# Kernel tuning notes

Hardware: AMD Instinct MI355X
Metric: run time of the kernel (lower is better)

Reference implementation:

```python
import jax, jax.numpy as jnp
import numpy as np

B, S, DIM = 2, 2048, 1024
N_HEAD, HEAD_DIM = 16, 64


def setup_inputs() -> dict:
    key = jax.random.key(0)
    k1, k2, k3, k4 = jax.random.split(key, 4)
    x = jax.random.normal(k1, (B, S, DIM), dtype=jnp.float32)
    # rotary table: cos/sin pairs, shape [S, head_dim//2, 2]
    half = HEAD_DIM // 2
    inv_freq = 1.0 / (10000.0 ** (jnp.arange(0, half, dtype=jnp.float32) / half))
    t = jnp.arange(S, dtype=jnp.float32)
    ang = t[:, None] * inv_freq[None, :]
    freqs_cis = jnp.stack([jnp.cos(ang), jnp.sin(ang)], axis=-1)  # [S, half, 2]
    # causal boolean mask [1,1,S,S] (True = attend)
    mask = jnp.tril(jnp.ones((S, S), dtype=bool))[None, None]
    wqkv = jax.random.normal(k2, (3 * DIM, DIM), dtype=jnp.float32) * (DIM ** -0.5)
    wo = jax.random.normal(k3, (DIM, DIM), dtype=jnp.float32) * (DIM ** -0.5)
    return {"x": x, "freqs_cis": freqs_cis, "mask": mask, "wqkv": wqkv, "wo": wo}


def apply_rotary_emb(x, freqs_cis):
    # x: [B, S, H, D]; freqs_cis: [S, D//2, 2]
    xs = x.reshape(*x.shape[:-1], -1, 2)  # [B,S,H,D//2,2]
    fc = freqs_cis[None, :, None, :, :]  # [1,S,1,D//2,2]
    xr, xi = xs[..., 0], xs[..., 1]
    cr, ci = fc[..., 0], fc[..., 1]
    out = jnp.stack([xr * cr - xi * ci, xi * cr + xr * ci], axis=-1)
    return out.reshape(x.shape)


def reference(x, freqs_cis, mask, wqkv, wo):
    bsz, seqlen, _ = x.shape
    qkv = jnp.einsum('bsd,ed->bse', x, wqkv)  # [B,S,3*dim]
    q, k, v = jnp.split(qkv, 3, axis=-1)
    q = q.reshape(bsz, seqlen, N_HEAD, HEAD_DIM)
    k = k.reshape(bsz, seqlen, N_HEAD, HEAD_DIM)
    v = v.reshape(bsz, seqlen, N_HEAD, HEAD_DIM)
    q = apply_rotary_emb(q, freqs_cis)
    k = apply_rotary_emb(k, freqs_cis)
    scale = HEAD_DIM ** -0.5
    scores = jnp.einsum('bqhd,bkhd->bhqk', q, k) * scale  # [B,H,S,S]
    scores = jnp.where(mask, scores, jnp.finfo(scores.dtype).min)
    attn = jax.nn.softmax(scores, axis=-1)
    y = jnp.einsum('bhqk,bkhd->bqhd', attn, v).reshape(bsz, seqlen, N_HEAD * HEAD_DIM)
    return jnp.einsum('bse,de->bsd', y, wo)
```

## Files before the change

### kernel.cpp

```cpp
#include <hip/hip_runtime.h>
#include <hip/hip_bf16.h>
#include <stdint.h>


typedef __attribute__((ext_vector_type(8))) __bf16 bf16x8;
typedef __attribute__((ext_vector_type(4))) float f32x4;
typedef __attribute__((ext_vector_type(16))) float f32x16;

union B8 { uint4 u; bf16x8 v; unsigned short us[8]; };

static __device__ __forceinline__ float bf2f(unsigned short u) {
  union { unsigned int ui; float f; } x; x.ui = ((unsigned int)u) << 16; return x.f;
}
static __device__ __forceinline__ unsigned short f2bf(float f) {
  union { float f; unsigned int ui; } x; x.f = f;
  unsigned int r = x.ui + 0x7fffu + ((x.ui >> 16) & 1u);
  return (unsigned short)(r >> 16);
}
static __device__ __forceinline__ unsigned int cvt_pk_bf16(float lo, float hi) {
  unsigned int r;
  asm("v_cvt_pk_bf16_f32 %0, %1, %2" : "=v"(r) : "v"(lo), "v"(hi));
  return r;
}
static __device__ __forceinline__ f32x4 mfma16(bf16x8 a, bf16x8 b, f32x4 c) {
  return __builtin_amdgcn_mfma_f32_16x16x32_bf16(a, b, c, 0, 0, 0);
}
static __device__ __forceinline__ f32x16 mfma32(bf16x8 a, bf16x8 b, f32x16 c) {
  return __builtin_amdgcn_mfma_f32_32x32x16_bf16(a, b, c, 0, 0, 0);
}
#define AS1 __attribute__((address_space(1)))
#define AS3 __attribute__((address_space(3)))
static __device__ __forceinline__ void gload_lds16(const void* g, void* l) {
  __builtin_amdgcn_global_load_lds((const AS1 unsigned int*)g,
                                   (AS3 unsigned int*)l, 16, 0, 0);
}

__global__ __launch_bounds__(256) void cvt_all_kernel(
    const float* __restrict__ x, const float* __restrict__ wqkv,
    const float* __restrict__ wo,
    unsigned short* __restrict__ xb, unsigned short* __restrict__ wqkvb,
    unsigned short* __restrict__ wob) {
  int i = blockIdx.x * 256 + threadIdx.x;
  const float* src; unsigned short* dst; int off;
  if (i < 1048576)       { src = x;    dst = xb;    off = i; }
  else if (i < 1835008)  { src = wqkv; dst = wqkvb; off = i - 1048576; }
  else                   { src = wo;   dst = wob;   off = i - 1835008; }
  float4 f = ((const float4*)src)[off];
  ushort4 u;
  u.x = f2bf(f.x); u.y = f2bf(f.y); u.z = f2bf(f.z); u.w = f2bf(f.w);
  ((ushort4*)dst)[off] = u;
}

__global__ __launch_bounds__(256) void qkv_rope_kernel(
    const unsigned short* __restrict__ xb,
    const unsigned short* __restrict__ wqkvb,
    const float* __restrict__ freqs,
    unsigned short* __restrict__ Q,
    unsigned short* __restrict__ K,
    unsigned short* __restrict__ Vt)
{
  __shared__ __align__(16) unsigned short As[128 * 64];
  __shared__ __align__(16) unsigned short Bs[128 * 64];
  const int t = threadIdx.x;
  const int lane = t & 63, wv = t >> 6;
  const int l31 = lane & 31, lh = lane >> 5;
  const int wm = wv >> 1, wn = wv & 1;
  const int tm = blockIdx.x & 31, tn = blockIdx.x >> 5;
  const int m0 = tm * 128, n0 = tn * 128;

  f32x16 acc[2][2] = {};

  for (int k0 = 0; k0 < 1024; k0 += 64) {
    for (int r = 0; r < 4; ++r) {
      int cid = t + 256 * r;
      int row = cid >> 3, jc = cid & 7;
      int sc = jc ^ (row & 7);
      gload_lds16(xb    + (size_t)(m0 + row) * 1024 + k0 + sc * 8, (char*)As + cid * 16);
      gload_lds16(wqkvb + (size_t)(n0 + row) * 1024 + k0 + sc * 8, (char*)Bs + cid * 16);
    }
    __syncthreads();
    for (int kst = 0; kst < 4; ++kst) {
      const int g = kst * 2 + lh;
      bf16x8 a[2], b[2];
      for (int s2 = 0; s2 < 2; ++s2) {
        int ra = wm * 64 + s2 * 32 + l31;
        a[s2] = *(const bf16x8*)((const char*)As + ra * 128 + (g ^ (ra & 7)) * 16);
        int rb = wn * 64 + s2 * 32 + l31;
        b[s2] = *(const bf16x8*)((const char*)Bs + rb * 128 + (g ^ (rb & 7)) * 16);
      }
      for (int sm = 0; sm < 2; ++sm)
        for (int sn = 0; sn < 2; ++sn)
          acc[sm][sn] = mfma32(a[sm], b[sn], acc[sm][sn]);
    }
    __syncthreads();
  }

  for (int sm = 0; sm < 2; ++sm) {
    for (int sn = 0; sn < 2; ++sn) {
      const int e = n0 + wn * 64 + sn * 32 + l31;
      const int seg = e >> 10;
      const int eh = e & 1023;
      const int h = eh >> 6, d = eh & 63;
      for (int r = 0; r < 16; ++r) {
        const int m = m0 + wm * 64 + sm * 32 + (r & 3) + 8 * (r >> 2) + 4 * lh;
        const int b_ = m >> 11, s_ = m & 2047;
        float v = acc[sm][sn][r];
        if (seg == 2) {
          Vt[((size_t)(b_ * 16 + h) * 64 + d) * 2048 + s_] = f2bf(v);
        } else {
          float partner = __shfl_xor(v, 1, 64);
          float2 fc = *(const float2*)(freqs + s_ * 64 + (d & ~1));
          float outv = (d & 1) ? (v * fc.x + partner * fc.y)
                               : (v * fc.x - partner * fc.y);
          unsigned short* dst = (seg == 0) ? Q : K;
          dst[((size_t)(b_ * 16 + h) * 2048 + s_) * 64 + d] = f2bf(outv);
        }
      }
    }
  }
}

struct QState {
  bf16x8 qf0, qf1;
  f32x4 o[4];
  float lp[4];
};

static __device__ __forceinline__ void load_q(QState& st,
    const unsigned short* Qb, int q0, int c, int quad) {
  st.qf0 = *(const bf16x8*)(Qb + (q0 + c) * 64 + quad * 8);
  st.qf1 = *(const bf16x8*)(Qb + (q0 + c) * 64 + 32 + quad * 8);
}

static __device__ __forceinline__ void attn_chunk(
    QState& st, const char* Ks, const char* Vs, unsigned short* myp,
    int c, int quad, int k0, int q0, bool diag)
{
  f32x4 sfr[4];
  for (int kc = 0; kc < 4; ++kc) {
    const int key = kc * 16 + c;
    const int s0 = quad ^ (key & 7), s1 = (4 + quad) ^ (key & 7);
    f32x4 sacc = {};
    sacc = mfma16(st.qf0, *(const bf16x8*)(Ks + key * 128 + s0 * 16), sacc);
    sacc = mfma16(st.qf1, *(const bf16x8*)(Ks + key * 128 + s1 * 16), sacc);
    sfr[kc] = sacc;
  }
  for (int i = 0; i < 4; ++i) {
    const int qrow = q0 + quad * 4 + i;
    float e[4];
    for (int kc = 0; kc < 4; ++kc) {
      float arg = fmaf(sfr[kc][i], 0.18033688f, -20.19773057f);
      if (diag && (k0 + kc * 16 + c > qrow)) arg = -1e30f;
      e[kc] = exp2f(arg);
    }
    st.lp[i] += (e[0] + e[1]) + (e[2] + e[3]);
    unsigned int u01 = cvt_pk_bf16(e[0], e[1]);
    unsigned int u23 = cvt_pk_bf16(e[2], e[3]);
    unsigned short* prow = myp + (quad * 4 + i) * 72;
    prow[c]      = (unsigned short)u01;
    prow[16 + c] = (unsigned short)(u01 >> 16);
    prow[32 + c] = (unsigned short)u23;
    prow[48 + c] = (unsigned short)(u23 >> 16);
  }
  bf16x8 pf[2];
  pf[0] = *(const bf16x8*)(myp + c * 72 + quad * 8);
  pf[1] = *(const bf16x8*)(myp + c * 72 + 32 + quad * 8);
  for (int ct = 0; ct < 4; ++ct) {
    const int d = ct * 16 + c;
    const int s0 = quad ^ (d & 7), s1 = (4 + quad) ^ (d & 7);
    st.o[ct] = mfma16(pf[0], *(const bf16x8*)(Vs + d * 128 + s0 * 16), st.o[ct]);
    st.o[ct] = mfma16(pf[1], *(const bf16x8*)(Vs + d * 128 + s1 * 16), st.o[ct]);
  }
}

__global__ __launch_bounds__(256) void attn_partial_kernel(
    const unsigned short* __restrict__ Q,
    const unsigned short* __restrict__ K,
    const unsigned short* __restrict__ Vt,
    unsigned short* __restrict__ Po,
    float* __restrict__ Pl)
{
  __shared__ __align__(16) unsigned short Ks[64 * 64];
  __shared__ __align__(16) unsigned short Vs[64 * 64];
  __shared__ __align__(16) unsigned short plds[4][16 * 72];
  const int t = threadIdx.x;
  const int lane = t & 63, wv = t >> 6;
  const int c = lane & 15, quad = lane >> 4;
  const int bh = blockIdx.x & 31;
  const int rest = blockIdx.x >> 5;
  const int j = rest >> 1, half = rest & 1;
  const int qA = j * 64 + wv * 16;
  const int qB = (31 - j) * 64 + wv * 16;

  const unsigned short* Qb = Q + (size_t)bh * (2048 * 64);
  const unsigned short* Kb = K + (size_t)bh * (2048 * 64);
  const unsigned short* Vb = Vt + (size_t)bh * (64 * 2048);

  QState A = {}, Bst = {};
  load_q(A, Qb, qA, c, quad);
  load_q(Bst, Qb, qB, c, quad);

  unsigned short* myp = plds[wv];
  const int ktmax = 31 - j;

  for (int kt = half; kt <= ktmax; kt += 2) {
    const int k0 = kt * 64;
    __syncthreads();
    for (int r = 0; r < 2; ++r) {
      int cid = t + 256 * r;
      int row = cid >> 3, jc = cid & 7;
      int sc = jc ^ (row & 7);
      gload_lds16(Kb + (size_t)(k0 + row) * 64 + sc * 8, (char*)Ks + cid * 16);
      gload_lds16(Vb + (size_t)row * 2048 + k0 + sc * 8, (char*)Vs + cid * 16);
    }
    __syncthreads();
    attn_chunk(Bst, (const char*)Ks, (const char*)Vs, myp, c, quad,
               k0, qB, kt == ktmax);
    if (kt <= j)
      attn_chunk(A, (const char*)Ks, (const char*)Vs, myp, c, quad,
                 k0, qA, kt == j);
  }

  unsigned short* Poh = Po + (size_t)half * (32 * 2048 * 64) + (size_t)bh * (2048 * 64);
  float* Plh = Pl + (size_t)half * (32 * 2048) + bh * 2048;
  for (int set = 0; set < 2; ++set) {
    QState& st = set ? Bst : A;
    const int q0 = set ? qB : qA;
    for (int i = 0; i < 4; ++i) {
      float l = st.lp[i];
      l += __shfl_xor(l, 1, 16);
      l += __shfl_xor(l, 2, 16);
      l += __shfl_xor(l, 4, 16);
      l += __shfl_xor(l, 8, 16);
      const int s = q0 + quad * 4 + i;
      for (int ct = 0; ct < 4; ++ct)
        Poh[(size_t)s * 64 + ct * 16 + c] = f2bf(st.o[ct][i]);
      if (c == 0) Plh[s] = l;
    }
  }
}

__global__ __launch_bounds__(256) void combine_kernel(
    const unsigned short* __restrict__ Po, const float* __restrict__ Pl,
    unsigned short* __restrict__ Yb)
{
  const int idx = blockIdx.x * 256 + threadIdx.x;
  const int bh = idx >> 14, rem = idx & 16383;
  const int s = rem >> 3, g = rem & 7;
  const size_t base = (size_t)bh * (2048 * 64) + (size_t)s * 64 + g * 8;
  B8 a, b;
  a.u = *(const uint4*)(Po + base);
  b.u = *(const uint4*)(Po + (size_t)(32 * 2048 * 64) + base);
  float l = Pl[bh * 2048 + s] + Pl[32 * 2048 + bh * 2048 + s];
  float inv = 1.0f / l;
  B8 y;
  for (int k = 0; k < 8; ++k)
    y.us[k] = f2bf((bf2f(a.us[k]) + bf2f(b.us[k])) * inv);
  const int b_ = bh >> 4, h = bh & 15;
  *(uint4*)(Yb + ((size_t)(b_ * 2048 + s)) * 1024 + h * 64 + g * 8) = y.u;
}

__global__ __launch_bounds__(256) void attn_kernel(
    const unsigned short* __restrict__ Q,
    const unsigned short* __restrict__ K,
    const unsigned short* __restrict__ Vt,
    unsigned short* __restrict__ Y)
{
  __shared__ __align__(16) unsigned short Ks[64 * 64];
  __shared__ __align__(16) unsigned short Vs[64 * 64];
  __shared__ __align__(16) unsigned short plds[4][16 * 72];
  const int t = threadIdx.x;
  const int lane = t & 63, wv = t >> 6;
  const int c = lane & 15, quad = lane >> 4;
  const int j = blockIdx.x >> 5, bh = blockIdx.x & 31;
  const int b = bh >> 4, h = bh & 15;
  const int qA = j * 64 + wv * 16;
  const int qB = (31 - j) * 64 + wv * 16;

  const unsigned short* Qb = Q + (size_t)bh * (2048 * 64);
  const unsigned short* Kb = K + (size_t)bh * (2048 * 64);
  const unsigned short* Vb = Vt + (size_t)bh * (64 * 2048);

  QState A = {}, Bst = {};
  load_q(A, Qb, qA, c, quad);
  load_q(Bst, Qb, qB, c, quad);

  const int nkt = 32 - j;
  unsigned short* myp = plds[wv];

  for (int kt = 0; kt < nkt; ++kt) {
    const int k0 = kt * 64;
    __syncthreads();
    for (int r = 0; r < 2; ++r) {
      int cid = t + 256 * r;
      int row = cid >> 3, jc = cid & 7;
      int sc = jc ^ (row & 7);
      gload_lds16(Kb + (size_t)(k0 + row) * 64 + sc * 8, (char*)Ks + cid * 16);
      gload_lds16(Vb + (size_t)row * 2048 + k0 + sc * 8, (char*)Vs + cid * 16);
    }
    __syncthreads();
    attn_chunk(Bst, (const char*)Ks, (const char*)Vs, myp, c, quad,
               k0, qB, kt == 31 - j);
    if (kt <= j)
      attn_chunk(A, (const char*)Ks, (const char*)Vs, myp, c, quad,
                 k0, qA, kt == j);
  }

  for (int set = 0; set < 2; ++set) {
    QState& st = set ? Bst : A;
    const int q0 = set ? qB : qA;
    for (int i = 0; i < 4; ++i) {
      float l = st.lp[i];
      l += __shfl_xor(l, 1, 16);
      l += __shfl_xor(l, 2, 16);
      l += __shfl_xor(l, 4, 16);
      l += __shfl_xor(l, 8, 16);
      float inv = 1.0f / l;
      const int s = q0 + quad * 4 + i;
      unsigned short* dst = Y + ((size_t)(b * 2048 + s)) * 1024 + h * 64;
      for (int ct = 0; ct < 4; ++ct)
        dst[ct * 16 + c] = f2bf(st.o[ct][i] * inv);
    }
  }
}

__global__ __launch_bounds__(256) void out_proj_kernel(
    const unsigned short* __restrict__ Y,
    const unsigned short* __restrict__ wob,
    float* __restrict__ out)
{
  __shared__ __align__(16) unsigned short As[128 * 64];
  __shared__ __align__(16) unsigned short Bs[64 * 64];
  const int t = threadIdx.x;
  const int lane = t & 63, wv = t >> 6;
  const int l31 = lane & 31, lh = lane >> 5;
  const int wm = wv >> 1, wn = wv & 1;
  const int tm = blockIdx.x & 31, tn = blockIdx.x >> 5;
  const int m0 = tm * 128, n0 = tn * 64;

  f32x16 acc[2] = {};

  for (int k0 = 0; k0 < 1024; k0 += 64) {
    for (int r = 0; r < 4; ++r) {
      int cid = t + 256 * r;
      int row = cid >> 3, jc = cid & 7;
      int sc = jc ^ (row & 7);
      gload_lds16(Y + (size_t)(m0 + row) * 1024 + k0 + sc * 8, (char*)As + cid * 16);
    }
    for (int r = 0; r < 2; ++r) {
      int cid = t + 256 * r;
      int row = cid >> 3, jc = cid & 7;
      int sc = jc ^ (row & 7);
      gload_lds16(wob + (size_t)(n0 + row) * 1024 + k0 + sc * 8, (char*)Bs + cid * 16);
    }
    __syncthreads();
    for (int kst = 0; kst < 4; ++kst) {
      const int g = kst * 2 + lh;
      bf16x8 a[2], b;
      for (int s2 = 0; s2 < 2; ++s2) {
        int ra = wm * 64 + s2 * 32 + l31;
        a[s2] = *(const bf16x8*)((const char*)As + ra * 128 + (g ^ (ra & 7)) * 16);
      }
      int rb = wn * 32 + l31;
      b = *(const bf16x8*)((const char*)Bs + rb * 128 + (g ^ (rb & 7)) * 16);
      acc[0] = mfma32(a[0], b, acc[0]);
      acc[1] = mfma32(a[1], b, acc[1]);
    }
    __syncthreads();
  }

  const int col = n0 + wn * 32 + l31;
  for (int sm = 0; sm < 2; ++sm)
    for (int r = 0; r < 16; ++r) {
      const int m = m0 + wm * 64 + sm * 32 + (r & 3) + 8 * (r >> 2) + 4 * lh;
      out[(size_t)m * 1024 + col] = acc[sm][r];
    }
}

extern "C" void kernel_launch(void* const* d_in, const int* in_sizes, int n_in,
                              void* d_out, int out_size, void* d_ws, size_t ws_size,
                              hipStream_t stream) {
  const float* x     = (const float*)d_in[0];
  const float* freqs = (const float*)d_in[1];
  const float* wqkv  = (const float*)d_in[3];
  const float* wo    = (const float*)d_in[4];
  float* out = (float*)d_out;

  const size_t BHSD = (size_t)2 * 16 * 2048 * 64;
  unsigned short* Q     = (unsigned short*)d_ws;
  unsigned short* K     = Q + BHSD;
  unsigned short* Vt    = K + BHSD;
  unsigned short* Yb    = Vt + BHSD;
  unsigned short* xb    = Yb + BHSD;
  unsigned short* wqkvb = xb + 4194304;
  unsigned short* wob   = wqkvb + 3145728;
  unsigned short* Po    = wob + 1048576;
  float*          Pl    = (float*)(Po + 2 * BHSD);

  const size_t need_fast =
      (size_t)((char*)(Pl + 2 * 32 * 2048) - (char*)d_ws);

  cvt_all_kernel<<<8192, 256, 0, stream>>>(x, wqkv, wo, xb, wqkvb, wob);
  qkv_rope_kernel<<<768, 256, 0, stream>>>(xb, wqkvb, freqs, Q, K, Vt);
  if (ws_size >= need_fast) {
    attn_partial_kernel<<<1024, 256, 0, stream>>>(Q, K, Vt, Po, Pl);
    combine_kernel<<<2048, 256, 0, stream>>>(Po, Pl, Yb);
  } else {
    attn_kernel<<<512, 256, 0, stream>>>(Q, K, Vt, Yb);
  }
  out_proj_kernel<<<512, 256, 0, stream>>>(Yb, wob, out);
}
```

Before: 210.1 us.

## Double-buffer LDS in QKV and out-proj GEMMs, widen QKV tile to 192 columns

Both GEMM kernels now stage the next K-slice into a second LDS buffer while computing on the current one, so each iteration needs only one barrier and global loads overlap with MFMA work. The QKV kernel moves to 384 threads (6 waves) with a 128x192 tile and 512 blocks. The out-projection remaps block indices so that neighbouring blocks share weight columns, which should improve L2 reuse. In exchange, LDS use per block roughly doubles or more, which can lower occupancy, and the new wave-to-tile mapping changes how the RoPE epilogue is laid out.

```diff
diff --git a/kernel.cpp b/kernel.cpp
--- a/kernel.cpp
+++ b/kernel.cpp
@@ -51,7 +51,7 @@
   ((ushort4*)dst)[off] = u;
 }
 
-__global__ __launch_bounds__(256) void qkv_rope_kernel(
+__global__ __launch_bounds__(384, 3) void qkv_rope_kernel(
     const unsigned short* __restrict__ xb,
     const unsigned short* __restrict__ wqkvb,
     const float* __restrict__ freqs,
@@ -59,40 +59,55 @@
     unsigned short* __restrict__ K,
     unsigned short* __restrict__ Vt)
 {
-  __shared__ __align__(16) unsigned short As[128 * 64];
-  __shared__ __align__(16) unsigned short Bs[128 * 64];
+  __shared__ __align__(16) unsigned short As[2][128 * 64];
+  __shared__ __align__(16) unsigned short Bs[2][192 * 64];
   const int t = threadIdx.x;
   const int lane = t & 63, wv = t >> 6;
   const int l31 = lane & 31, lh = lane >> 5;
-  const int wm = wv >> 1, wn = wv & 1;
+  const int wm = wv & 1, wn = wv >> 1;
   const int tm = blockIdx.x & 31, tn = blockIdx.x >> 5;
-  const int m0 = tm * 128, n0 = tn * 128;
+  const int m0 = tm * 128, n0 = tn * 192;
 
   f32x16 acc[2][2] = {};
 
+  auto stage = [&](int bb, int k0) {
+    for (int r = 0; r < 7; ++r) {
+      int cid = t + 384 * r;
+      if (cid < 1024) {
+        int row = cid >> 3, jc = cid & 7, sc = jc ^ (row & 7);
+        gload_lds16(xb + (size_t)(m0 + row) * 1024 + k0 + sc * 8,
+                    (char*)As[bb] + cid * 16);
+      } else if (cid < 2560) {
+        int c2 = cid - 1024;
+        int row = c2 >> 3, jc = c2 & 7, sc = jc ^ (row & 7);
+        gload_lds16(wqkvb + (size_t)(n0 + row) * 1024 + k0 + sc * 8,
+                    (char*)Bs[bb] + c2 * 16);
+      }
+    }
+  };
+
+  stage(0, 0);
+  __syncthreads();
+  int cur = 0;
   for (int k0 = 0; k0 < 1024; k0 += 64) {
-    for (int r = 0; r < 4; ++r) {
-      int cid = t + 256 * r;
-      int row = cid >> 3, jc = cid & 7;
-      int sc = jc ^ (row & 7);
-      gload_lds16(xb    + (size_t)(m0 + row) * 1024 + k0 + sc * 8, (char*)As + cid * 16);
-      gload_lds16(wqkvb + (size_t)(n0 + row) * 1024 + k0 + sc * 8, (char*)Bs + cid * 16);
-    }
-    __syncthreads();
+    if (k0 + 64 < 1024) stage(cur ^ 1, k0 + 64);
+    const char* Ap = (const char*)As[cur];
+    const char* Bp = (const char*)Bs[cur];
     for (int kst = 0; kst < 4; ++kst) {
       const int g = kst * 2 + lh;
       bf16x8 a[2], b[2];
       for (int s2 = 0; s2 < 2; ++s2) {
         int ra = wm * 64 + s2 * 32 + l31;
-        a[s2] = *(const bf16x8*)((const char*)As + ra * 128 + (g ^ (ra & 7)) * 16);
+        a[s2] = *(const bf16x8*)(Ap + ra * 128 + (g ^ (ra & 7)) * 16);
         int rb = wn * 64 + s2 * 32 + l31;
-        b[s2] = *(const bf16x8*)((const char*)Bs + rb * 128 + (g ^ (rb & 7)) * 16);
+        b[s2] = *(const bf16x8*)(Bp + rb * 128 + (g ^ (rb & 7)) * 16);
       }
       for (int sm = 0; sm < 2; ++sm)
         for (int sn = 0; sn < 2; ++sn)
           acc[sm][sn] = mfma32(a[sm], b[sn], acc[sm][sn]);
     }
     __syncthreads();
+    cur ^= 1;
   }
 
   for (int sm = 0; sm < 2; ++sm) {
@@ -329,44 +344,56 @@
     const unsigned short* __restrict__ wob,
     float* __restrict__ out)
 {
-  __shared__ __align__(16) unsigned short As[128 * 64];
-  __shared__ __align__(16) unsigned short Bs[64 * 64];
+  __shared__ __align__(16) unsigned short As[2][128 * 64];
+  __shared__ __align__(16) unsigned short Bs[2][64 * 64];
   const int t = threadIdx.x;
   const int lane = t & 63, wv = t >> 6;
   const int l31 = lane & 31, lh = lane >> 5;
   const int wm = wv >> 1, wn = wv & 1;
-  const int tm = blockIdx.x & 31, tn = blockIdx.x >> 5;
+  const int blk = blockIdx.x;
+  const int tm = (blk & 7) * 4 + ((blk >> 3) & 3);
+  const int tn = blk >> 5;
   const int m0 = tm * 128, n0 = tn * 64;
 
   f32x16 acc[2] = {};
 
+  auto stage = [&](int bb, int k0) {
+    for (int r = 0; r < 6; ++r) {
+      int cid = t + 256 * r;
+      if (cid < 1024) {
+        int row = cid >> 3, jc = cid & 7, sc = jc ^ (row & 7);
+        gload_lds16(Y + (size_t)(m0 + row) * 1024 + k0 + sc * 8,
+                    (char*)As[bb] + cid * 16);
+      } else {
+        int c2 = cid - 1024;
+        int row = c2 >> 3, jc = c2 & 7, sc = jc ^ (row & 7);
+        gload_lds16(wob + (size_t)(n0 + row) * 1024 + k0 + sc * 8,
+                    (char*)Bs[bb] + c2 * 16);
+      }
+    }
+  };
+
+  stage(0, 0);
+  __syncthreads();
+  int cur = 0;
   for (int k0 = 0; k0 < 1024; k0 += 64) {
-    for (int r = 0; r < 4; ++r) {
-      int cid = t + 256 * r;
-      int row = cid >> 3, jc = cid & 7;
-      int sc = jc ^ (row & 7);
-      gload_lds16(Y + (size_t)(m0 + row) * 1024 + k0 + sc * 8, (char*)As + cid * 16);
-    }
-    for (int r = 0; r < 2; ++r) {
-      int cid = t + 256 * r;
-      int row = cid >> 3, jc = cid & 7;
-      int sc = jc ^ (row & 7);
-      gload_lds16(wob + (size_t)(n0 + row) * 1024 + k0 + sc * 8, (char*)Bs + cid * 16);
-    }
-    __syncthreads();
+    if (k0 + 64 < 1024) stage(cur ^ 1, k0 + 64);
+    const char* Ap = (const char*)As[cur];
+    const char* Bp = (const char*)Bs[cur];
     for (int kst = 0; kst < 4; ++kst) {
       const int g = kst * 2 + lh;
       bf16x8 a[2], b;
       for (int s2 = 0; s2 < 2; ++s2) {
         int ra = wm * 64 + s2 * 32 + l31;
-        a[s2] = *(const bf16x8*)((const char*)As + ra * 128 + (g ^ (ra & 7)) * 16);
+        a[s2] = *(const bf16x8*)(Ap + ra * 128 + (g ^ (ra & 7)) * 16);
       }
       int rb = wn * 32 + l31;
-      b = *(const bf16x8*)((const char*)Bs + rb * 128 + (g ^ (rb & 7)) * 16);
+      b = *(const bf16x8*)(Bp + rb * 128 + (g ^ (rb & 7)) * 16);
       acc[0] = mfma32(a[0], b, acc[0]);
       acc[1] = mfma32(a[1], b, acc[1]);
     }
     __syncthreads();
+    cur ^= 1;
   }
 
   const int col = n0 + wn * 32 + l31;
@@ -401,7 +428,7 @@
       (size_t)((char*)(Pl + 2 * 32 * 2048) - (char*)d_ws);
 
   cvt_all_kernel<<<8192, 256, 0, stream>>>(x, wqkv, wo, xb, wqkvb, wob);
-  qkv_rope_kernel<<<768, 256, 0, stream>>>(xb, wqkvb, freqs, Q, K, Vt);
+  qkv_rope_kernel<<<512, 384, 0, stream>>>(xb, wqkvb, freqs, Q, K, Vt);
   if (ws_size >= need_fast) {
     attn_partial_kernel<<<1024, 256, 0, stream>>>(Q, K, Vt, Po, Pl);
     combine_kernel<<<2048, 256, 0, stream>>>(Po, Pl, Yb);
```

Result: slower. 242.6 us (+15.5%).
